# Kernel tuning notes

Measured on AMD Instinct MI355X. Metric: run time of the kernel, lower is better.

Reference implementation:

```python
import jax, jax.numpy as jnp
import numpy as np

N_NODES = 100000
N_EDGES = 1600000
IN_FEATS = 64
OUT_FEATS = 64


def setup_inputs() -> dict:
    key = jax.random.key(0)
    k1, k2, k3, k4 = jax.random.split(key, 4)
    features = jax.random.normal(k1, (N_NODES, IN_FEATS), dtype=jnp.float32)
    src = jax.random.randint(k2, (N_EDGES,), 0, N_NODES, dtype=jnp.int32)
    dst = jax.random.randint(k3, (N_EDGES,), 0, N_NODES, dtype=jnp.int32)
    # Linear(in_feats, out_feats): W is [out, in] like torch, b is [out]
    W = jax.random.normal(k4, (OUT_FEATS, IN_FEATS), dtype=jnp.float32) * (1.0 / np.sqrt(IN_FEATS))
    b = jnp.zeros((OUT_FEATS,), dtype=jnp.float32)
    return {"features": features, "src": src, "dst": dst, "W": W, "b": b}


def reference(features, src, dst, W, b):
    # update_all(copy_src('h','m'), sum('m','h')): for each edge, message = h[src],
    # aggregated by sum at dst. Equivalent to a segment-sum scatter-add.
    msgs = features[src]  # [E, in_feats] gather
    agg = jax.ops.segment_sum(msgs, dst, num_segments=N_NODES)  # [N, in_feats]
    # NodeUpdateModule: Linear + relu (dropout=0 so no dropout path)
    h = jnp.einsum('ni,oi->no', agg, W) + b
    return jax.nn.relu(h)
```

## Files before the change

### kernel.cpp

```cpp
#include <hip/hip_runtime.h>

#define N_NODES 100000
#define N_EDGES 1600000
#define TILES 6250

#define NPB 128
#define NB 782
#define SUBS 256
#define CAP 14
#define OVF_CAP 16384
#define LOVF_CAP 512
#define LISTCAP 3712

typedef __attribute__((ext_vector_type(8))) short short8;
typedef __attribute__((ext_vector_type(4))) float f32x4;

static __device__ __forceinline__ unsigned short f2bf(float f) {
    unsigned int u = __float_as_uint(f);
    unsigned int r = (u + 0x7fffu + ((u >> 16) & 1u)) >> 16;
    return (unsigned short)r;
}
static __device__ __forceinline__ float bfl(unsigned int u) {
    return __uint_as_float(u << 16);
}
static __device__ __forceinline__ float bfh(unsigned int u) {
    return __uint_as_float(u & 0xffff0000u);
}

__global__ __launch_bounds__(256) void gcn_gemm(
    const float* __restrict__ feat, const float* __restrict__ W,
    unsigned int* __restrict__ g32) {
    int l = threadIdx.x & 63, wv = threadIdx.x >> 6;
    int r = l & 15, c = l >> 4;

    short8 bf[4][2];
#pragma unroll
    for (int t = 0; t < 4; ++t)
#pragma unroll
        for (int s = 0; s < 2; ++s) {
            const float* wp = W + (16 * t + r) * 64 + 32 * s + c * 8;
            float4 w0 = *(const float4*)wp;
            float4 w1 = *(const float4*)(wp + 4);
            short8 f;
            f[0] = (short)f2bf(w0.x); f[1] = (short)f2bf(w0.y);
            f[2] = (short)f2bf(w0.z); f[3] = (short)f2bf(w0.w);
            f[4] = (short)f2bf(w1.x); f[5] = (short)f2bf(w1.y);
            f[6] = (short)f2bf(w1.z); f[7] = (short)f2bf(w1.w);
            bf[t][s] = f;
        }

    int tile0 = (blockIdx.x * 4 + wv) * 4;
#pragma unroll
    for (int ti = 0; ti < 4; ++ti) {
        int tile = tile0 + ti;
        if (tile >= TILES) break;
        int m0 = tile * 16;
        f32x4 acc0 = {0,0,0,0}, acc1 = {0,0,0,0}, acc2 = {0,0,0,0}, acc3 = {0,0,0,0};
#pragma unroll
        for (int s = 0; s < 2; ++s) {
            const float* ap = feat + (m0 + r) * 64 + 32 * s + c * 8;
            float4 a0 = *(const float4*)ap;
            float4 a1 = *(const float4*)(ap + 4);
            short8 af;
            af[0] = (short)f2bf(a0.x); af[1] = (short)f2bf(a0.y);
            af[2] = (short)f2bf(a0.z); af[3] = (short)f2bf(a0.w);
            af[4] = (short)f2bf(a1.x); af[5] = (short)f2bf(a1.y);
            af[6] = (short)f2bf(a1.z); af[7] = (short)f2bf(a1.w);
            acc0 = __builtin_amdgcn_mfma_f32_16x16x32_bf16(af, bf[0][s], acc0, 0, 0, 0);
            acc1 = __builtin_amdgcn_mfma_f32_16x16x32_bf16(af, bf[1][s], acc1, 0, 0, 0);
            acc2 = __builtin_amdgcn_mfma_f32_16x16x32_bf16(af, bf[2][s], acc2, 0, 0, 0);
            acc3 = __builtin_amdgcn_mfma_f32_16x16x32_bf16(af, bf[3][s], acc3, 0, 0, 0);
        }
#pragma unroll
        for (int t = 0; t < 4; ++t) {
            f32x4 a = (t == 0) ? acc0 : (t == 1) ? acc1 : (t == 2) ? acc2 : acc3;
#pragma unroll
            for (int reg = 0; reg < 4; ++reg) {
                float d = a[reg];
                float o = __shfl_xor(d, 1);
                if (!(l & 1)) {
                    int m = m0 + c * 4 + reg;
                    int n = 16 * t + r;
                    g32[(m * 64 + n) >> 1] =
                        (unsigned int)f2bf(d) | ((unsigned int)f2bf(o) << 16);
                }
            }
        }
    }
}

__global__ __launch_bounds__(1024) void gcn_bin(
    const int* __restrict__ src, const int* __restrict__ dst,
    unsigned int* __restrict__ cursor, unsigned int* __restrict__ region,
    unsigned int* __restrict__ ovf_cnt, uint2* __restrict__ ovf) {
    __shared__ unsigned int cnt[NB];
    __shared__ unsigned int data[NB][CAP];
    __shared__ uint2 lovf[LOVF_CAP];
    __shared__ unsigned int lovf_n, lovf_base;
    int sub = blockIdx.x;
    int tid = threadIdx.x;
    for (int i = tid; i < NB; i += 1024) cnt[i] = 0;
    if (tid == 0) lovf_n = 0;
    __syncthreads();

    int base = sub * (N_EDGES / SUBS);
    int end = base + (N_EDGES / SUBS);
    int i = base + tid;
    int s = 0, d = 0;
    if (i < end) { s = src[i]; d = dst[i]; }
    while (i < end) {
        int inext = i + 1024;
        int sn = 0, dn = 0;
        if (inext < end) { sn = src[inext]; dn = dst[inext]; }
        int bk = d >> 7;
        unsigned int c = atomicAdd(&cnt[bk], 1u);
        if (c < CAP) {
            data[bk][c] = ((unsigned int)(d & 127) << 17) | (unsigned int)s;
        } else {
            unsigned int o = atomicAdd(&lovf_n, 1u);
            if (o < LOVF_CAP) lovf[o] = make_uint2((unsigned int)s, (unsigned int)d);
        }
        i = inext; s = sn; d = dn;
    }
    __syncthreads();

    unsigned int rbase = (unsigned int)sub * NB * CAP;
    for (int idx = tid; idx < NB * CAP; idx += 1024) {
        int bk = idx / CAP, slot = idx - bk * CAP;
        unsigned int c = cnt[bk];
        if (slot < (int)(c < CAP ? c : CAP))
            region[rbase + (unsigned int)idx] = data[bk][slot];
    }
    for (int bk = tid; bk < NB; bk += 1024)
        cursor[sub * NB + bk] = cnt[bk];

    unsigned int n = lovf_n < LOVF_CAP ? lovf_n : LOVF_CAP;
    if (tid == 0) lovf_base = atomicAdd(ovf_cnt, n);
    __syncthreads();
    for (unsigned int t = tid; t < n; t += 1024) {
        unsigned int p = lovf_base + t;
        if (p < OVF_CAP) ovf[p] = lovf[t];
    }
}

__global__ __launch_bounds__(512) void gcn_gather3(
    const uint2* __restrict__ g64, const unsigned int* __restrict__ cursor,
    const unsigned int* __restrict__ region, const unsigned int* __restrict__ ovf_cnt,
    const uint2* __restrict__ ovf, const float* __restrict__ bias,
    float* __restrict__ out) {
    __shared__ unsigned int list[LISTCAP];
    __shared__ unsigned int sorted[LISTCAP];
    __shared__ unsigned int scnt[SUBS], soff[SUBS];
    __shared__ unsigned int cnt2[NPB], off2[NPB], cur2[NPB];
    __shared__ unsigned int ltot;

    int b = blockIdx.x;
    int tid = threadIdx.x;

    if (tid < SUBS) {
        unsigned int c = cursor[(unsigned)tid * NB + b];
        scnt[tid] = c < CAP ? c : CAP;
    }
    if (tid < NPB) cnt2[tid] = 0;
    __syncthreads();
    if (tid < SUBS) soff[tid] = scnt[tid];
    __syncthreads();
    for (int off = 1; off < SUBS; off <<= 1) {
        unsigned int t = 0;
        if (tid < SUBS && tid >= off) t = soff[tid - off];
        __syncthreads();
        if (tid < SUBS) soff[tid] += t;
        __syncthreads();
    }
    if (tid == 0) ltot = soff[SUBS - 1];
    __syncthreads();

    for (int idx = tid; idx < SUBS * CAP; idx += 512) {
        int s = idx / CAP, slot = idx - s * CAP;
        if (slot < (int)scnt[s])
            list[soff[s] - scnt[s] + slot] =
                region[((unsigned)s * NB + b) * CAP + slot];
    }
    unsigned int oc = *ovf_cnt;
    if (oc > OVF_CAP) oc = OVF_CAP;
    for (unsigned int i = tid; i < oc; i += 512) {
        uint2 e = ovf[i];
        if ((int)(e.y >> 7) == b) {
            unsigned int p = atomicAdd(&ltot, 1u);
            if (p < LISTCAP) list[p] = ((e.y & 127u) << 17) | e.x;
        }
    }
    __syncthreads();
    unsigned int T = ltot < LISTCAP ? ltot : LISTCAP;

    for (unsigned int i = tid; i < T; i += 512)
        atomicAdd(&cnt2[list[i] >> 17], 1u);
    __syncthreads();
    if (tid < NPB) off2[tid] = cnt2[tid];
    __syncthreads();
    for (int off = 1; off < NPB; off <<= 1) {
        unsigned int t = 0;
        if (tid < NPB && tid >= off) t = off2[tid - off];
        __syncthreads();
        if (tid < NPB) off2[tid] += t;
        __syncthreads();
    }
    if (tid < NPB) cur2[tid] = off2[tid] - cnt2[tid];
    __syncthreads();
    for (unsigned int i = tid; i < T; i += 512) {
        unsigned int v = list[i];
        unsigned int p = atomicAdd(&cur2[v >> 17], 1u);
        if (p < LISTCAP) sorted[p] = v & 0x1FFFFu;
    }
    __syncthreads();

    int wv = tid >> 6, l = tid & 63, grp = l >> 4, k = l & 15;
#pragma unroll
    for (int nb = 0; nb < 4; ++nb) {
        int dl = wv * 16 + nb * 4 + grp;
        int node = b * NPB + dl;
        if (node < N_NODES) {
            unsigned int start = off2[dl] - cnt2[dl];
            int cnt = (int)cnt2[dl];
            float a0 = 0.f, a1 = 0.f, a2 = 0.f, a3 = 0.f;
#pragma unroll 4
            for (int j = 0; j < cnt; ++j) {
                unsigned int s0 = sorted[start + j];
                uint2 w = g64[s0 * 16 + k];
                a0 += bfl(w.x); a1 += bfh(w.x); a2 += bfl(w.y); a3 += bfh(w.y);
            }
            float4 b4 = *(const float4*)(bias + 4 * k);
            float4 o;
            o.x = fmaxf(a0 + b4.x, 0.0f);
            o.y = fmaxf(a1 + b4.y, 0.0f);
            o.z = fmaxf(a2 + b4.z, 0.0f);
            o.w = fmaxf(a3 + b4.w, 0.0f);
            *(float4*)(out + node * 64 + 4 * k) = o;
        }
    }
}

extern "C" void kernel_launch(void* const* d_in, const int* in_sizes, int n_in,
                              void* d_out, int out_size, void* d_ws, size_t ws_size,
                              hipStream_t stream) {
    const float* features = (const float*)d_in[0];
    const int*   src      = (const int*)d_in[1];
    const int*   dst      = (const int*)d_in[2];
    const float* W        = (const float*)d_in[3];
    const float* b        = (const float*)d_in[4];
    float* out = (float*)d_out;

    unsigned int* ws     = (unsigned int*)d_ws;
    unsigned int* cursor = ws;
    unsigned int* ovfcnt = ws + 200192;
    uint2*        ovf    = (uint2*)(ws + 200256);
    unsigned int* region = ws + 233024;
    unsigned int* g32    = ws + 3035712;

    hipMemsetAsync(ovfcnt, 0, 64 * sizeof(unsigned int), stream);

    gcn_gemm<<<(TILES + 15) / 16, 256, 0, stream>>>(features, W, g32);
    gcn_bin<<<SUBS, 1024, 0, stream>>>(src, dst, cursor, region, ovfcnt, ovf);
    gcn_gather3<<<NB, 512, 0, stream>>>((const uint2*)g32, cursor, region,
                                        ovfcnt, ovf, b, out);
}
```

Baseline: 79.23 us.

## Fuse GEMM and edge binning into one launch, add nontemporal loads/stores

Merges the bf16 MFMA feature-transform kernel and the edge-binning kernel into one grid, with extra blocks (1024 threads, 16 waves each) doing the GEMM tiles. This removes a kernel launch and lets the two independent phases run at the same time. The region reads and output writes in the gather kernel become nontemporal, and the gather loop unroll goes from 4 to 8. The GEMM blocks now reserve the same large shared-memory footprint as the binning blocks, which may limit how many blocks fit per CU.

```diff
diff --git a/kernel.cpp b/kernel.cpp
--- a/kernel.cpp
+++ b/kernel.cpp
@@ -11,6 +11,7 @@
 #define OVF_CAP 16384
 #define LOVF_CAP 512
 #define LISTCAP 3712
+#define GEMM_BLKS 98
 
 typedef __attribute__((ext_vector_type(8))) short short8;
 typedef __attribute__((ext_vector_type(4))) float f32x4;
@@ -27,69 +28,9 @@
     return __uint_as_float(u & 0xffff0000u);
 }
 
-__global__ __launch_bounds__(256) void gcn_gemm(
+__global__ __launch_bounds__(1024) void gcn_prep(
     const float* __restrict__ feat, const float* __restrict__ W,
-    unsigned int* __restrict__ g32) {
-    int l = threadIdx.x & 63, wv = threadIdx.x >> 6;
-    int r = l & 15, c = l >> 4;
-
-    short8 bf[4][2];
-#pragma unroll
-    for (int t = 0; t < 4; ++t)
-#pragma unroll
-        for (int s = 0; s < 2; ++s) {
-            const float* wp = W + (16 * t + r) * 64 + 32 * s + c * 8;
-            float4 w0 = *(const float4*)wp;
-            float4 w1 = *(const float4*)(wp + 4);
-            short8 f;
-            f[0] = (short)f2bf(w0.x); f[1] = (short)f2bf(w0.y);
-            f[2] = (short)f2bf(w0.z); f[3] = (short)f2bf(w0.w);
-            f[4] = (short)f2bf(w1.x); f[5] = (short)f2bf(w1.y);
-            f[6] = (short)f2bf(w1.z); f[7] = (short)f2bf(w1.w);
-            bf[t][s] = f;
-        }
-
-    int tile0 = (blockIdx.x * 4 + wv) * 4;
-#pragma unroll
-    for (int ti = 0; ti < 4; ++ti) {
-        int tile = tile0 + ti;
-        if (tile >= TILES) break;
-        int m0 = tile * 16;
-        f32x4 acc0 = {0,0,0,0}, acc1 = {0,0,0,0}, acc2 = {0,0,0,0}, acc3 = {0,0,0,0};
-#pragma unroll
-        for (int s = 0; s < 2; ++s) {
-            const float* ap = feat + (m0 + r) * 64 + 32 * s + c * 8;
-            float4 a0 = *(const float4*)ap;
-            float4 a1 = *(const float4*)(ap + 4);
-            short8 af;
-            af[0] = (short)f2bf(a0.x); af[1] = (short)f2bf(a0.y);
-            af[2] = (short)f2bf(a0.z); af[3] = (short)f2bf(a0.w);
-            af[4] = (short)f2bf(a1.x); af[5] = (short)f2bf(a1.y);
-            af[6] = (short)f2bf(a1.z); af[7] = (short)f2bf(a1.w);
-            acc0 = __builtin_amdgcn_mfma_f32_16x16x32_bf16(af, bf[0][s], acc0, 0, 0, 0);
-            acc1 = __builtin_amdgcn_mfma_f32_16x16x32_bf16(af, bf[1][s], acc1, 0, 0, 0);
-            acc2 = __builtin_amdgcn_mfma_f32_16x16x32_bf16(af, bf[2][s], acc2, 0, 0, 0);
-            acc3 = __builtin_amdgcn_mfma_f32_16x16x32_bf16(af, bf[3][s], acc3, 0, 0, 0);
-        }
-#pragma unroll
-        for (int t = 0; t < 4; ++t) {
-            f32x4 a = (t == 0) ? acc0 : (t == 1) ? acc1 : (t == 2) ? acc2 : acc3;
-#pragma unroll
-            for (int reg = 0; reg < 4; ++reg) {
-                float d = a[reg];
-                float o = __shfl_xor(d, 1);
-                if (!(l & 1)) {
-                    int m = m0 + c * 4 + reg;
-                    int n = 16 * t + r;
-                    g32[(m * 64 + n) >> 1] =
-                        (unsigned int)f2bf(d) | ((unsigned int)f2bf(o) << 16);
-                }
-            }
-        }
-    }
-}
-
-__global__ __launch_bounds__(1024) void gcn_bin(
+    unsigned int* __restrict__ g32,
     const int* __restrict__ src, const int* __restrict__ dst,
     unsigned int* __restrict__ cursor, unsigned int* __restrict__ region,
     unsigned int* __restrict__ ovf_cnt, uint2* __restrict__ ovf) {
@@ -97,8 +38,71 @@
     __shared__ unsigned int data[NB][CAP];
     __shared__ uint2 lovf[LOVF_CAP];
     __shared__ unsigned int lovf_n, lovf_base;
+
+    int tid = threadIdx.x;
+    if (blockIdx.x >= SUBS) {
+        int b = blockIdx.x - SUBS;
+        int l = tid & 63, wv = tid >> 6;
+        int r = l & 15, c = l >> 4;
+
+        short8 bfr[4][2];
+#pragma unroll
+        for (int t = 0; t < 4; ++t)
+#pragma unroll
+            for (int s = 0; s < 2; ++s) {
+                const float* wp = W + (16 * t + r) * 64 + 32 * s + c * 8;
+                float4 w0 = *(const float4*)wp;
+                float4 w1 = *(const float4*)(wp + 4);
+                short8 f;
+                f[0] = (short)f2bf(w0.x); f[1] = (short)f2bf(w0.y);
+                f[2] = (short)f2bf(w0.z); f[3] = (short)f2bf(w0.w);
+                f[4] = (short)f2bf(w1.x); f[5] = (short)f2bf(w1.y);
+                f[6] = (short)f2bf(w1.z); f[7] = (short)f2bf(w1.w);
+                bfr[t][s] = f;
+            }
+
+        int tile0 = (b * 16 + wv) * 4;
+#pragma unroll
+        for (int ti = 0; ti < 4; ++ti) {
+            int tile = tile0 + ti;
+            if (tile >= TILES) break;
+            int m0 = tile * 16;
+            f32x4 acc0 = {0,0,0,0}, acc1 = {0,0,0,0}, acc2 = {0,0,0,0}, acc3 = {0,0,0,0};
+#pragma unroll
+            for (int s = 0; s < 2; ++s) {
+                const float* ap = feat + (m0 + r) * 64 + 32 * s + c * 8;
+                float4 a0 = *(const float4*)ap;
+                float4 a1 = *(const float4*)(ap + 4);
+                short8 af;
+                af[0] = (short)f2bf(a0.x); af[1] = (short)f2bf(a0.y);
+                af[2] = (short)f2bf(a0.z); af[3] = (short)f2bf(a0.w);
+                af[4] = (short)f2bf(a1.x); af[5] = (short)f2bf(a1.y);
+                af[6] = (short)f2bf(a1.z); af[7] = (short)f2bf(a1.w);
+                acc0 = __builtin_amdgcn_mfma_f32_16x16x32_bf16(af, bfr[0][s], acc0, 0, 0, 0);
+                acc1 = __builtin_amdgcn_mfma_f32_16x16x32_bf16(af, bfr[1][s], acc1, 0, 0, 0);
+                acc2 = __builtin_amdgcn_mfma_f32_16x16x32_bf16(af, bfr[2][s], acc2, 0, 0, 0);
+                acc3 = __builtin_amdgcn_mfma_f32_16x16x32_bf16(af, bfr[3][s], acc3, 0, 0, 0);
+            }
+#pragma unroll
+            for (int t = 0; t < 4; ++t) {
+                f32x4 a = (t == 0) ? acc0 : (t == 1) ? acc1 : (t == 2) ? acc2 : acc3;
+#pragma unroll
+                for (int reg = 0; reg < 4; ++reg) {
+                    float dv = a[reg];
+                    float o = __shfl_xor(dv, 1);
+                    if (!(l & 1)) {
+                        int m = m0 + c * 4 + reg;
+                        int n = 16 * t + r;
+                        g32[(m * 64 + n) >> 1] =
+                            (unsigned int)f2bf(dv) | ((unsigned int)f2bf(o) << 16);
+                    }
+                }
+            }
+        }
+        return;
+    }
+
     int sub = blockIdx.x;
-    int tid = threadIdx.x;
     for (int i = tid; i < NB; i += 1024) cnt[i] = 0;
     if (tid == 0) lovf_n = 0;
     __syncthreads();
@@ -179,7 +183,7 @@
         int s = idx / CAP, slot = idx - s * CAP;
         if (slot < (int)scnt[s])
             list[soff[s] - scnt[s] + slot] =
-                region[((unsigned)s * NB + b) * CAP + slot];
+                __builtin_nontemporal_load(&region[((unsigned)s * NB + b) * CAP + slot]);
     }
     unsigned int oc = *ovf_cnt;
     if (oc > OVF_CAP) oc = OVF_CAP;
@@ -223,19 +227,19 @@
             unsigned int start = off2[dl] - cnt2[dl];
             int cnt = (int)cnt2[dl];
             float a0 = 0.f, a1 = 0.f, a2 = 0.f, a3 = 0.f;
-#pragma unroll 4
+#pragma unroll 8
             for (int j = 0; j < cnt; ++j) {
                 unsigned int s0 = sorted[start + j];
                 uint2 w = g64[s0 * 16 + k];
                 a0 += bfl(w.x); a1 += bfh(w.x); a2 += bfl(w.y); a3 += bfh(w.y);
             }
             float4 b4 = *(const float4*)(bias + 4 * k);
-            float4 o;
+            f32x4 o;
             o.x = fmaxf(a0 + b4.x, 0.0f);
             o.y = fmaxf(a1 + b4.y, 0.0f);
             o.z = fmaxf(a2 + b4.z, 0.0f);
             o.w = fmaxf(a3 + b4.w, 0.0f);
-            *(float4*)(out + node * 64 + 4 * k) = o;
+            __builtin_nontemporal_store(o, (f32x4*)(out + node * 64 + 4 * k));
         }
     }
 }
@@ -257,10 +261,10 @@
     unsigned int* region = ws + 233024;
     unsigned int* g32    = ws + 3035712;
 
-    hipMemsetAsync(ovfcnt, 0, 64 * sizeof(unsigned int), stream);
-
-    gcn_gemm<<<(TILES + 15) / 16, 256, 0, stream>>>(features, W, g32);
-    gcn_bin<<<SUBS, 1024, 0, stream>>>(src, dst, cursor, region, ovfcnt, ovf);
+    (void)hipMemsetAsync(ovfcnt, 0, 64 * sizeof(unsigned int), stream);
+
+    gcn_prep<<<SUBS + GEMM_BLKS, 1024, 0, stream>>>(
+        features, W, g32, src, dst, cursor, region, ovfcnt, ovf);
     gcn_gather3<<<NB, 512, 0, stream>>>((const uint2*)g32, cursor, region,
                                         ovfcnt, ovf, b, out);
 }
```

New measurement: 80.64 us. Within noise of the previous version (+1.8%).
